# Optimization experiments

Measured on AMD Instinct MI355X. Metric: run time of the kernel, lower is better.

The kernel has to match this reference:

```python
import jax, jax.numpy as jnp
import numpy as np

# cfg constants (from init_kwargs)
RBF_START = 0.0
RBF_END = 10.0
RBF_STEPS = 32
ENERGY_SCALE = 1.0
EPS = 1e-10

L, R, E, F, P = 64, 4096, 32, 64, 8


def setup_inputs() -> dict:
    key = jax.random.key(0)
    ks = jax.random.split(key, 6)
    return {
        "lig_feat": jax.random.normal(ks[0], (L, E, F), dtype=jnp.float32),
        "rec_feat": jax.random.normal(ks[1], (R, E, F), dtype=jnp.float32),
        "lig_coords": jax.random.normal(ks[2], (P, L, 3), dtype=jnp.float32),
        "rec_coord": jax.random.normal(ks[3], (R, 3), dtype=jnp.float32),
        "weight": jax.random.normal(ks[4], (), dtype=jnp.float32),
        "bias": jax.random.normal(ks[5], (), dtype=jnp.float32),
    }


def reference(lig_feat, rec_feat, lig_coords, rec_coord, weight, bias):
    # attention coefficients: [L, R, E]
    atn = jnp.einsum('lef,ref->lre', lig_feat, rec_feat)
    mu = jnp.linspace(RBF_START, RBF_END, RBF_STEPS, dtype=jnp.float32)  # [E]
    sigma = (RBF_START - RBF_END) / RBF_STEPS

    def energy(lig_coord):  # lig_coord: [L, 3]
        # cdist_diff: eps added per-coordinate before sum, as in the torch code
        diff = lig_coord[:, None, :] - rec_coord[None, :, :]      # [L, R, 3]
        dists = jnp.sqrt(((diff * diff) + EPS).sum(-1))            # [L, R]
        z = (dists[..., None] - mu) / sigma                        # [L, R, E]
        rbfs = jnp.exp(-(z * z))
        return (atn * rbfs * ENERGY_SCALE).sum()

    Us = jax.vmap(energy)(lig_coords)  # [P]
    # ScaleOutput
    return Us * weight + bias
```

## Files before the change

kernel.cpp:

```cpp
#include <hip/hip_runtime.h>

#define NL 64
#define NR 4096
#define NE 32
#define NF 64
#define NP 8

#define DSCALE 3.8435917081166390f
#define MUSTEP 1.2398683f
#define EPS3   3e-10f

typedef _Float16 f16x8 __attribute__((ext_vector_type(8)));
typedef float    f32x4 __attribute__((ext_vector_type(4)));

#define LIG_B 0
#define REC_B 32768
#define NBLK  2048

__global__ __launch_bounds__(256, 4)
void ff_main(const float* __restrict__ lig_feat,
             const float* __restrict__ rec_feat,
             const float* __restrict__ lig_coords,
             const float* __restrict__ rec_coord,
             float* __restrict__ ws)
{
    __shared__ __align__(16) char smem[40960];

    const int t    = threadIdx.x;
    const int bid  = blockIdx.x;
    const int rb   = bid & 255;
    const int eb   = bid >> 8;
    const int r0   = rb * 16;
    const int e0   = eb * 4;
    const int lane = t & 63;
    const int wv   = t >> 6;
    const int l0   = wv * 16;
    const int cn   = lane & 15;
    const int kg   = lane >> 4;

#pragma unroll
    for (int j = 0; j < 4; ++j) {
        const int idx = j * 256 + t;
        const int e = idx >> 8, r = (idx >> 4) & 15, fq = idx & 15;
        const float4 v = *(const float4*)&rec_feat[((r0 + r) * NE + e0 + e) * NF + fq * 4];
        union { _Float16 h[4]; uint2 u; } pk;
        pk.h[0] = (_Float16)v.x; pk.h[1] = (_Float16)v.y;
        pk.h[2] = (_Float16)v.z; pk.h[3] = (_Float16)v.w;
        *(uint2*)(smem + REC_B + e * 2048 + r * 128 + ((8 * fq) ^ ((r & 7) << 4))) = pk.u;
    }
#pragma unroll 8
    for (int j = 0; j < 16; ++j) {
        const int idx = j * 256 + t;
        const int e = idx >> 10, rem = idx & 1023, l = rem >> 4, fq = rem & 15;
        const float4 v = *(const float4*)&lig_feat[(l * NE + e0 + e) * NF + fq * 4];
        union { _Float16 h[4]; uint2 u; } pk;
        pk.h[0] = (_Float16)v.x; pk.h[1] = (_Float16)v.y;
        pk.h[2] = (_Float16)v.z; pk.h[3] = (_Float16)v.w;
        *(uint2*)(smem + LIG_B + e * 8192 + l * 128 + ((8 * fq) ^ ((l & 7) << 4))) = pk.u;
    }

    const int rr = r0 + cn;
    const float rx = rec_coord[rr * 3 + 0];
    const float ry = rec_coord[rr * 3 + 1];
    const float rz = rec_coord[rr * 3 + 2];
    float ds[4][NP];
#pragma unroll
    for (int reg = 0; reg < 4; ++reg) {
        const int l = l0 + kg * 4 + reg;
#pragma unroll
        for (int p = 0; p < NP; ++p) {
            const float lx = lig_coords[(p * NL + l) * 3 + 0];
            const float ly = lig_coords[(p * NL + l) * 3 + 1];
            const float lz = lig_coords[(p * NL + l) * 3 + 2];
            const float dx = lx - rx, dy = ly - ry, dz = lz - rz;
            const float d2 = fmaf(dx, dx, fmaf(dy, dy, fmaf(dz, dz, EPS3)));
            ds[reg][p] = __builtin_amdgcn_sqrtf(d2) * DSCALE;
        }
    }

    __syncthreads();

    const int sx = (cn & 7) << 4;
    const int a_row = LIG_B + (l0 + cn) * 128;
    const int b_row = REC_B + cn * 128;
    const int a0o = a_row + ((kg * 16) ^ sx);
    const int a1o = a_row + ((kg * 16 + 64) ^ sx);
    const int b0o = b_row + ((kg * 16) ^ sx);
    const int b1o = b_row + ((kg * 16 + 64) ^ sx);

    float U[NP];
#pragma unroll
    for (int p = 0; p < NP; ++p) U[p] = 0.f;

#pragma unroll
    for (int ee = 0; ee < 4; ++ee) {
        const f16x8 a0 = *(const f16x8*)(smem + a0o + ee * 8192);
        const f16x8 a1 = *(const f16x8*)(smem + a1o + ee * 8192);
        const f16x8 b0 = *(const f16x8*)(smem + b0o + ee * 2048);
        const f16x8 b1 = *(const f16x8*)(smem + b1o + ee * 2048);
        f32x4 C = {0.f, 0.f, 0.f, 0.f};
        C = __builtin_amdgcn_mfma_f32_16x16x32_f16(a0, b0, C, 0, 0, 0);
        C = __builtin_amdgcn_mfma_f32_16x16x32_f16(a1, b1, C, 0, 0, 0);

        const float mu = (float)(e0 + ee) * MUSTEP;
#pragma unroll
        for (int reg = 0; reg < 4; ++reg) {
            const float a = C[reg];
#pragma unroll
            for (int p = 0; p < NP; ++p) {
                const float z = ds[reg][p] - mu;
                U[p] = fmaf(a, __builtin_amdgcn_exp2f(-(z * z)), U[p]);
            }
        }
    }

#pragma unroll
    for (int p = 0; p < NP; ++p) {
        float v = U[p];
        for (int off = 32; off; off >>= 1) v += __shfl_down(v, off, 64);
        U[p] = v;
    }
    __syncthreads();
    float* wred = (float*)smem;
    if (lane == 0) {
#pragma unroll
        for (int p = 0; p < NP; ++p) wred[wv * 8 + p] = U[p];
    }
    __syncthreads();
    if (t < NP)
        ws[t * NBLK + bid] = wred[t] + wred[8 + t] + wred[16 + t] + wred[24 + t];
}

__global__ __launch_bounds__(512)
void ff_fin(const float* __restrict__ ws,
            const float* __restrict__ w,
            const float* __restrict__ b,
            float* __restrict__ out) {
    const int t = threadIdx.x, lane = t & 63, p = t >> 6;
    float s = 0.f;
#pragma unroll
    for (int j = 0; j < NBLK / 64; ++j) s += ws[p * NBLK + j * 64 + lane];
    for (int off = 32; off; off >>= 1) s += __shfl_down(s, off, 64);
    if (lane == 0) out[p] = fmaf(s, w[0], b[0]);
}

extern "C" void kernel_launch(void* const* d_in, const int* in_sizes, int n_in,
                              void* d_out, int out_size, void* d_ws, size_t ws_size,
                              hipStream_t stream) {
    const float* lig_feat   = (const float*)d_in[0];
    const float* rec_feat   = (const float*)d_in[1];
    const float* lig_coords = (const float*)d_in[2];
    const float* rec_coord  = (const float*)d_in[3];
    const float* weight     = (const float*)d_in[4];
    const float* bias       = (const float*)d_in[5];
    float* out = (float*)d_out;
    float* ws  = (float*)d_ws;

    hipLaunchKernelGGL(ff_main, dim3(NBLK), dim3(256), 0, stream,
                       lig_feat, rec_feat, lig_coords, rec_coord, ws);
    hipLaunchKernelGGL(ff_fin, dim3(1), dim3(512), 0, stream,
                       ws, weight, bias, out);
}
```

Baseline: 28.23 us.

## Precompute fp16 distance table in separate kernel and read lig features directly

Adds a kernel that computes all scaled ligand-receptor distances for every pose once and stores them as packed fp16 in workspace. The main kernel then loads this table instead of recomputing 8 sqrt per element in each of 8 e-blocks. The main kernel also stops staging ligand features in shared memory and reads them from global straight into MFMA operands, cutting LDS from 40KB to 8KB. The final reduction is vectorised. This costs an extra launch, a 4MB table write and read, and fp16 rounding of distances, which may hurt accuracy because the Gaussian is sensitive to distance error.

```diff
diff --git a/kernel.cpp b/kernel.cpp
--- a/kernel.cpp
+++ b/kernel.cpp
@@ -11,20 +11,47 @@
 #define EPS3   3e-10f
 
 typedef _Float16 f16x8 __attribute__((ext_vector_type(8)));
+typedef __fp16   h16x2 __attribute__((ext_vector_type(2)));
 typedef float    f32x4 __attribute__((ext_vector_type(4)));
 
-#define LIG_B 0
-#define REC_B 32768
-#define NBLK  2048
+#define NBLK   2048
+#define DS_TAB_BYTES (NL * NR * NP * 2)
+
+__global__ __launch_bounds__(256)
+void ff_dist(const float* __restrict__ lig_coords,
+             const float* __restrict__ rec_coord,
+             void* __restrict__ ws)
+{
+    const int tid = blockIdx.x * 256 + threadIdx.x;
+    const int l = tid >> 12;
+    const int r = tid & 4095;
+    const float rx = rec_coord[r * 3 + 0];
+    const float ry = rec_coord[r * 3 + 1];
+    const float rz = rec_coord[r * 3 + 2];
+    float d[NP];
+#pragma unroll
+    for (int p = 0; p < NP; ++p) {
+        const float lx = lig_coords[(p * NL + l) * 3 + 0];
+        const float ly = lig_coords[(p * NL + l) * 3 + 1];
+        const float lz = lig_coords[(p * NL + l) * 3 + 2];
+        const float dx = lx - rx, dy = ly - ry, dz = lz - rz;
+        const float d2 = fmaf(dx, dx, fmaf(dy, dy, fmaf(dz, dz, EPS3)));
+        d[p] = __builtin_amdgcn_sqrtf(d2) * DSCALE;
+    }
+    union { h16x2 h[4]; uint4 u; } pk;
+#pragma unroll
+    for (int q = 0; q < 4; ++q)
+        pk.h[q] = __builtin_amdgcn_cvt_pkrtz(d[2 * q], d[2 * q + 1]);
+    ((uint4*)ws)[tid] = pk.u;
+}
 
 __global__ __launch_bounds__(256, 4)
 void ff_main(const float* __restrict__ lig_feat,
              const float* __restrict__ rec_feat,
-             const float* __restrict__ lig_coords,
-             const float* __restrict__ rec_coord,
-             float* __restrict__ ws)
+             void* __restrict__ ws)
 {
-    __shared__ __align__(16) char smem[40960];
+    __shared__ __align__(16) char recs[8192];
+    __shared__ float wred[32];
 
     const int t    = threadIdx.x;
     const int bid  = blockIdx.x;
@@ -38,55 +65,34 @@
     const int cn   = lane & 15;
     const int kg   = lane >> 4;
 
+    const int srow = t >> 4, sf = (t & 15) * 4;
+    const int swz = (8 * (t & 15)) ^ ((srow & 7) << 4);
 #pragma unroll
-    for (int j = 0; j < 4; ++j) {
-        const int idx = j * 256 + t;
-        const int e = idx >> 8, r = (idx >> 4) & 15, fq = idx & 15;
-        const float4 v = *(const float4*)&rec_feat[((r0 + r) * NE + e0 + e) * NF + fq * 4];
-        union { _Float16 h[4]; uint2 u; } pk;
-        pk.h[0] = (_Float16)v.x; pk.h[1] = (_Float16)v.y;
-        pk.h[2] = (_Float16)v.z; pk.h[3] = (_Float16)v.w;
-        *(uint2*)(smem + REC_B + e * 2048 + r * 128 + ((8 * fq) ^ ((r & 7) << 4))) = pk.u;
-    }
-#pragma unroll 8
-    for (int j = 0; j < 16; ++j) {
-        const int idx = j * 256 + t;
-        const int e = idx >> 10, rem = idx & 1023, l = rem >> 4, fq = rem & 15;
-        const float4 v = *(const float4*)&lig_feat[(l * NE + e0 + e) * NF + fq * 4];
-        union { _Float16 h[4]; uint2 u; } pk;
-        pk.h[0] = (_Float16)v.x; pk.h[1] = (_Float16)v.y;
-        pk.h[2] = (_Float16)v.z; pk.h[3] = (_Float16)v.w;
-        *(uint2*)(smem + LIG_B + e * 8192 + l * 128 + ((8 * fq) ^ ((l & 7) << 4))) = pk.u;
+    for (int e = 0; e < 4; ++e) {
+        const float4 v = *(const float4*)&rec_feat[((r0 + srow) * NE + e0 + e) * NF + sf];
+        union { h16x2 h[2]; uint2 u; } pk;
+        pk.h[0] = __builtin_amdgcn_cvt_pkrtz(v.x, v.y);
+        pk.h[1] = __builtin_amdgcn_cvt_pkrtz(v.z, v.w);
+        *(uint2*)(recs + e * 2048 + srow * 128 + swz) = pk.u;
     }
 
-    const int rr = r0 + cn;
-    const float rx = rec_coord[rr * 3 + 0];
-    const float ry = rec_coord[rr * 3 + 1];
-    const float rz = rec_coord[rr * 3 + 2];
+    const uint4* dtab = (const uint4*)ws;
     float ds[4][NP];
 #pragma unroll
     for (int reg = 0; reg < 4; ++reg) {
-        const int l = l0 + kg * 4 + reg;
+        union { uint4 u; _Float16 h[8]; } pk;
+        pk.u = dtab[(l0 + kg * 4 + reg) * NR + r0 + cn];
 #pragma unroll
-        for (int p = 0; p < NP; ++p) {
-            const float lx = lig_coords[(p * NL + l) * 3 + 0];
-            const float ly = lig_coords[(p * NL + l) * 3 + 1];
-            const float lz = lig_coords[(p * NL + l) * 3 + 2];
-            const float dx = lx - rx, dy = ly - ry, dz = lz - rz;
-            const float d2 = fmaf(dx, dx, fmaf(dy, dy, fmaf(dz, dz, EPS3)));
-            ds[reg][p] = __builtin_amdgcn_sqrtf(d2) * DSCALE;
-        }
+        for (int p = 0; p < NP; ++p) ds[reg][p] = (float)pk.h[p];
     }
 
     __syncthreads();
 
-    const int sx = (cn & 7) << 4;
-    const int a_row = LIG_B + (l0 + cn) * 128;
-    const int b_row = REC_B + cn * 128;
-    const int a0o = a_row + ((kg * 16) ^ sx);
-    const int a1o = a_row + ((kg * 16 + 64) ^ sx);
-    const int b0o = b_row + ((kg * 16) ^ sx);
-    const int b1o = b_row + ((kg * 16 + 64) ^ sx);
+    const int bsw = (cn & 7) << 4;
+    const int b_row = cn * 128;
+    const int b0o = b_row + ((kg * 16) ^ bsw);
+    const int b1o = b_row + ((kg * 16 + 64) ^ bsw);
+    const float* ligb = &lig_feat[((l0 + cn) * NE + e0) * NF + kg * 8];
 
     float U[NP];
 #pragma unroll
@@ -94,13 +100,24 @@
 
 #pragma unroll
     for (int ee = 0; ee < 4; ++ee) {
-        const f16x8 a0 = *(const f16x8*)(smem + a0o + ee * 8192);
-        const f16x8 a1 = *(const f16x8*)(smem + a1o + ee * 8192);
-        const f16x8 b0 = *(const f16x8*)(smem + b0o + ee * 2048);
-        const f16x8 b1 = *(const f16x8*)(smem + b1o + ee * 2048);
+        const float4 af0 = *(const float4*)(ligb + ee * NF + 0);
+        const float4 af1 = *(const float4*)(ligb + ee * NF + 4);
+        const float4 af2 = *(const float4*)(ligb + ee * NF + 32);
+        const float4 af3 = *(const float4*)(ligb + ee * NF + 36);
+        union { h16x2 h[4]; f16x8 v; } a0, a1;
+        a0.h[0] = __builtin_amdgcn_cvt_pkrtz(af0.x, af0.y);
+        a0.h[1] = __builtin_amdgcn_cvt_pkrtz(af0.z, af0.w);
+        a0.h[2] = __builtin_amdgcn_cvt_pkrtz(af1.x, af1.y);
+        a0.h[3] = __builtin_amdgcn_cvt_pkrtz(af1.z, af1.w);
+        a1.h[0] = __builtin_amdgcn_cvt_pkrtz(af2.x, af2.y);
+        a1.h[1] = __builtin_amdgcn_cvt_pkrtz(af2.z, af2.w);
+        a1.h[2] = __builtin_amdgcn_cvt_pkrtz(af3.x, af3.y);
+        a1.h[3] = __builtin_amdgcn_cvt_pkrtz(af3.z, af3.w);
+        const f16x8 b0 = *(const f16x8*)(recs + ee * 2048 + b0o);
+        const f16x8 b1 = *(const f16x8*)(recs + ee * 2048 + b1o);
         f32x4 C = {0.f, 0.f, 0.f, 0.f};
-        C = __builtin_amdgcn_mfma_f32_16x16x32_f16(a0, b0, C, 0, 0, 0);
-        C = __builtin_amdgcn_mfma_f32_16x16x32_f16(a1, b1, C, 0, 0, 0);
+        C = __builtin_amdgcn_mfma_f32_16x16x32_f16(a0.v, b0, C, 0, 0, 0);
+        C = __builtin_amdgcn_mfma_f32_16x16x32_f16(a1.v, b1, C, 0, 0, 0);
 
         const float mu = (float)(e0 + ee) * MUSTEP;
 #pragma unroll
@@ -121,25 +138,29 @@
         U[p] = v;
     }
     __syncthreads();
-    float* wred = (float*)smem;
     if (lane == 0) {
 #pragma unroll
         for (int p = 0; p < NP; ++p) wred[wv * 8 + p] = U[p];
     }
     __syncthreads();
+    float* wsP = (float*)((char*)ws + DS_TAB_BYTES);
     if (t < NP)
-        ws[t * NBLK + bid] = wred[t] + wred[8 + t] + wred[16 + t] + wred[24 + t];
+        wsP[t * NBLK + bid] = wred[t] + wred[8 + t] + wred[16 + t] + wred[24 + t];
 }
 
 __global__ __launch_bounds__(512)
-void ff_fin(const float* __restrict__ ws,
+void ff_fin(const void* __restrict__ ws,
             const float* __restrict__ w,
             const float* __restrict__ b,
             float* __restrict__ out) {
+    const float* wsP = (const float*)((const char*)ws + DS_TAB_BYTES);
     const int t = threadIdx.x, lane = t & 63, p = t >> 6;
     float s = 0.f;
 #pragma unroll
-    for (int j = 0; j < NBLK / 64; ++j) s += ws[p * NBLK + j * 64 + lane];
+    for (int j = 0; j < NBLK / 256; ++j) {
+        const float4 v = *(const float4*)&wsP[p * NBLK + j * 256 + lane * 4];
+        s += (v.x + v.y) + (v.z + v.w);
+    }
     for (int off = 32; off; off >>= 1) s += __shfl_down(s, off, 64);
     if (lane == 0) out[p] = fmaf(s, w[0], b[0]);
 }
@@ -154,10 +175,11 @@
     const float* weight     = (const float*)d_in[4];
     const float* bias       = (const float*)d_in[5];
     float* out = (float*)d_out;
-    float* ws  = (float*)d_ws;
 
+    hipLaunchKernelGGL(ff_dist, dim3(1024), dim3(256), 0, stream,
+                       lig_coords, rec_coord, d_ws);
     hipLaunchKernelGGL(ff_main, dim3(NBLK), dim3(256), 0, stream,
-                       lig_feat, rec_feat, lig_coords, rec_coord, ws);
+                       lig_feat, rec_feat, d_ws);
     hipLaunchKernelGGL(ff_fin, dim3(1), dim3(512), 0, stream,
-                       ws, weight, bias, out);
+                       d_ws, weight, bias, out);
 }
```

Result: slower. 33.85 us (+19.9%).
